# Kernel optimization log

Measured on AMD Instinct MI355X. Metric: run time of the kernel, lower is better.

## Reference

```python
import jax, jax.numpy as jnp
import numpy as np

B, N_ATOMS = 8192, 64      # molecules, atoms per molecule
DIM, EXTRA, N_CLS = 70, 7, 11
N_FP = 10000               # fingerprint vocab


def setup_inputs() -> dict:
    key = jax.random.key(0)
    ks = jax.random.split(key, 9)
    atoms = jax.random.randint(ks[0], (B, N_ATOMS), 0, N_FP, dtype=jnp.int64 if jax.config.jax_enable_x64 else jnp.int32)
    adjacency = jax.random.uniform(ks[1], (B, N_ATOMS, N_ATOMS), dtype=jnp.float32)
    sel_desc = jax.random.normal(ks[2], (B, EXTRA), dtype=jnp.float32)
    embed_table = jax.random.normal(ks[3], (N_FP, DIM), dtype=jnp.float32)
    w1 = jax.random.normal(ks[4], (DIM, DIM), dtype=jnp.float32) * 0.05
    b1 = jax.random.normal(ks[5], (DIM,), dtype=jnp.float32) * 0.05
    w2 = jax.random.normal(ks[6], (DIM, DIM), dtype=jnp.float32) * 0.05
    b2 = jax.random.normal(ks[7], (DIM,), dtype=jnp.float32) * 0.05
    wp = jax.random.normal(ks[8], (DIM + EXTRA, N_CLS), dtype=jnp.float32) * 0.05
    bp = jnp.zeros((N_CLS,), dtype=jnp.float32)
    return {"atoms": atoms, "adjacency": adjacency, "sel_desc": sel_desc,
            "embed_table": embed_table, "w1": w1, "b1": b1,
            "w2": w2, "b2": b2, "wp": wp, "bp": bp}


def reference(atoms, adjacency, sel_desc, embed_table, w1, b1, w2, b2, wp, bp):
    # embed atoms: [B, n, dim]
    x = embed_table[atoms]
    # message-passing layers: relu(linear) then (block-diagonal == batched) adjacency matmul
    for w, b in ((w1, b1), (w2, b2)):
        h = jax.nn.relu(jnp.einsum('bnd,de->bne', x, w) + b)
        x = jnp.einsum('bnm,bmd->bnd', adjacency, h)
    # segment-sum pool over atoms per molecule (sum_axis)
    y = jnp.sum(x, axis=1)                       # [B, dim]
    y = jnp.concatenate([y, sel_desc], axis=1)   # [B, dim+extra]
    return jnp.einsum('bd,dc->bc', y, wp) + bp   # [B, 11]
```

## Files before the change

kernel.cpp:

```cpp
#include <hip/hip_runtime.h>
#include <hip/hip_bf16.h>

#define NFP   10000
#define DIM   70
#define GPAD  72
#define NATOMS 64

typedef short  short8  __attribute__((ext_vector_type(8)));
typedef float  floatx4 __attribute__((ext_vector_type(4)));

__device__ inline unsigned short f2bf(float f) {
  union { float f; unsigned u; } x; x.f = f;
  unsigned r = x.u + 0x7fffu + ((x.u >> 16) & 1u);
  return (unsigned short)(r >> 16);
}

__device__ inline ushort2 pk2bf(float a, float b) {
  __hip_bfloat162 h = __float22bfloat162_rn(make_float2(a, b));
  union { __hip_bfloat162 h; ushort2 u; } c; c.h = h; return c.u;
}

__global__ __launch_bounds__(256) void precompute_G(
    const float* __restrict__ emb, const float* __restrict__ w1,
    const float* __restrict__ b1,  const float* __restrict__ w2,
    unsigned short* __restrict__ G) {
  __shared__ float w1s[DIM * GPAD];
  __shared__ float w2s[DIM * GPAD];
  __shared__ float b1s[GPAD];
  __shared__ float embs[32 * GPAD];
  __shared__ float e1s[32 * GPAD];
  const int t = threadIdx.x;

  for (int i = t; i < DIM * GPAD; i += 256) {
    int r = i / GPAD, c = i % GPAD;
    float v1 = 0.f, v2 = 0.f;
    if (c < DIM) { v1 = w1[r * DIM + c]; v2 = w2[r * DIM + c]; }
    w1s[i] = v1; w2s[i] = v2;
  }
  if (t < GPAD) b1s[t] = (t < DIM) ? b1[t] : 0.f;
  const int row0 = blockIdx.x * 32;
  for (int i = t; i < 32 * GPAD; i += 256) {
    int r = i / GPAD, c = i % GPAD;
    int vr = row0 + r;
    embs[i] = (vr < NFP && c < DIM) ? emb[vr * DIM + c] : 0.f;
  }
  __syncthreads();

  for (int task = t; task < 32 * 18; task += 256) {
    int r = task / 18, c4 = (task % 18) * 4;
    float4 acc = *(const float4*)&b1s[c4];
    for (int k = 0; k < DIM; k++) {
      float e = embs[r * GPAD + k];
      float4 w = *(const float4*)&w1s[k * GPAD + c4];
      acc.x = fmaf(e, w.x, acc.x); acc.y = fmaf(e, w.y, acc.y);
      acc.z = fmaf(e, w.z, acc.z); acc.w = fmaf(e, w.w, acc.w);
    }
    acc.x = fmaxf(acc.x, 0.f); acc.y = fmaxf(acc.y, 0.f);
    acc.z = fmaxf(acc.z, 0.f); acc.w = fmaxf(acc.w, 0.f);
    *(float4*)&e1s[r * GPAD + c4] = acc;
  }
  __syncthreads();

  for (int task = t; task < 32 * 18; task += 256) {
    int r = task / 18, c4 = (task % 18) * 4;
    int vr = row0 + r;
    if (vr >= NFP) continue;
    float ax = 0.f, ay = 0.f, az = 0.f, aw = 0.f;
    for (int k = 0; k < DIM; k++) {
      float e = e1s[r * GPAD + k];
      float4 w = *(const float4*)&w2s[k * GPAD + c4];
      ax = fmaf(e, w.x, ax); ay = fmaf(e, w.y, ay);
      az = fmaf(e, w.z, az); aw = fmaf(e, w.w, aw);
    }
    unsigned short* gp = G + vr * GPAD + c4;
    gp[0] = f2bf(ax); gp[1] = f2bf(ay); gp[2] = f2bf(az); gp[3] = f2bf(aw);
  }
}

__global__ __launch_bounds__(256, 6) void mol_fused(
    const int* __restrict__ atoms, const float* __restrict__ adj,
    const float* __restrict__ sel, const float* __restrict__ b2,
    const float* __restrict__ wp,  const float* __restrict__ bp,
    const unsigned short* __restrict__ G, float* __restrict__ out) {
  __shared__ unsigned short gTs[80 * GPAD];
  __shared__ float cpart[4 * 64];
  __shared__ float b2p[80];
  __shared__ float wps[77 * 11];
  __shared__ float bps[11];
  __shared__ float yacc[4 * 80];
  __shared__ float yv[80];

  const int b = blockIdx.x;
  const int t = threadIdx.x;
  const int w = t >> 6, lane = t & 63;
  const int q = lane >> 4, li = lane & 15;
  const int R = w * 16;

  const float* rp = adj + (size_t)b * 4096 + (R + li) * 64;
  float4 v0 = *(const float4*)(rp + q * 8);
  float4 v1 = *(const float4*)(rp + q * 8 + 4);
  float4 v2 = *(const float4*)(rp + 32 + q * 8);
  float4 v3 = *(const float4*)(rp + 36 + q * 8);
  union { short8 s; ushort2 u[4]; } A0, A1;
  A0.u[0] = pk2bf(v0.x, v0.y); A0.u[1] = pk2bf(v0.z, v0.w);
  A0.u[2] = pk2bf(v1.x, v1.y); A0.u[3] = pk2bf(v1.z, v1.w);
  A1.u[0] = pk2bf(v2.x, v2.y); A1.u[1] = pk2bf(v2.z, v2.w);
  A1.u[2] = pk2bf(v3.x, v3.y); A1.u[3] = pk2bf(v3.z, v3.w);
  {
    float c[16] = {v0.x, v0.y, v0.z, v0.w, v1.x, v1.y, v1.z, v1.w,
                   v2.x, v2.y, v2.z, v2.w, v3.x, v3.y, v3.z, v3.w};
#pragma unroll
    for (int m = 1; m <= 8; m <<= 1)
#pragma unroll
      for (int i = 0; i < 16; i++) c[i] += __shfl_xor(c[i], m);
    if (li == 0) {
      float* cp = &cpart[w * 64];
      *(float4*)&cp[q * 8]      = make_float4(c[0], c[1], c[2], c[3]);
      *(float4*)&cp[q * 8 + 4]  = make_float4(c[4], c[5], c[6], c[7]);
      *(float4*)&cp[32 + q * 8]     = make_float4(c[8],  c[9],  c[10], c[11]);
      *(float4*)&cp[32 + q * 8 + 4] = make_float4(c[12], c[13], c[14], c[15]);
    }
  }

  for (int i = t; i < 77 * 11; i += 256) wps[i] = wp[i];
  if (t < 11) bps[t] = bp[t];
  if (t < 80) b2p[t] = (t < DIM) ? b2[t] : 0.f;

  {
    const uint4* Gv = (const uint4*)G;
    const int p = t & 31;
    int2 aidx = *(const int2*)(atoms + b * 64 + 2 * p);
    int ch = t >> 5;
#pragma unroll
    for (int pass = 0; pass < 2; pass++) {
      if (pass == 1) { if (t >= 32) break; ch = 8; }
      uint4 g0 = Gv[(unsigned)aidx.x * 9 + ch];
      uint4 g1 = Gv[(unsigned)aidx.y * 9 + ch];
      unsigned base = (unsigned)(ch * 8) * GPAD + 2 * p;
      unsigned* d0 = (unsigned*)&gTs[base];
      d0[0 * (GPAD / 2) * 0] = 0;
      *(unsigned*)&gTs[base + 0 * GPAD] = (g0.x & 0xffffu) | (g1.x << 16);
      *(unsigned*)&gTs[base + 1 * GPAD] = (g0.x >> 16) | (g1.x & 0xffff0000u);
      *(unsigned*)&gTs[base + 2 * GPAD] = (g0.y & 0xffffu) | (g1.y << 16);
      *(unsigned*)&gTs[base + 3 * GPAD] = (g0.y >> 16) | (g1.y & 0xffff0000u);
      *(unsigned*)&gTs[base + 4 * GPAD] = (g0.z & 0xffffu) | (g1.z << 16);
      *(unsigned*)&gTs[base + 5 * GPAD] = (g0.z >> 16) | (g1.z & 0xffff0000u);
      *(unsigned*)&gTs[base + 6 * GPAD] = (g0.w & 0xffffu) | (g1.w << 16);
      *(unsigned*)&gTs[base + 7 * GPAD] = (g0.w >> 16) | (g1.w & 0xffff0000u);
    }
  }
  if (t < 72) {
    uint4 zz; zz.x = zz.y = zz.z = zz.w = 0u;
    *(uint4*)&gTs[72 * GPAD + t * 8] = zz;
  }
  __syncthreads();

  float cr[4];
#pragma unroll
  for (int r = 0; r < 4; r++) {
    int m = R + q * 4 + r;
    cr[r] = cpart[m] + cpart[64 + m] + cpart[128 + m] + cpart[192 + m];
  }

  floatx4 acc[5];
#pragma unroll
  for (int nt = 0; nt < 5; nt++) {
    floatx4 z = {0.f, 0.f, 0.f, 0.f};
    short8 b0 = *(const short8*)&gTs[(nt * 16 + li) * GPAD + q * 8];
    short8 b1 = *(const short8*)&gTs[(nt * 16 + li) * GPAD + 32 + q * 8];
    z = __builtin_amdgcn_mfma_f32_16x16x32_bf16(A0.s, b0, z, 0, 0, 0);
    z = __builtin_amdgcn_mfma_f32_16x16x32_bf16(A1.s, b1, z, 0, 0, 0);
    acc[nt] = z;
  }

  float ps[5];
#pragma unroll
  for (int nt = 0; nt < 5; nt++) {
    float bb = b2p[nt * 16 + li];
    float p = 0.f;
#pragma unroll
    for (int r = 0; r < 4; r++)
      p = fmaf(cr[r], fmaxf(acc[nt][r] + bb, 0.f), p);
    p += __shfl_xor(p, 16);
    p += __shfl_xor(p, 32);
    ps[nt] = p;
  }
  if (q == 0) {
#pragma unroll
    for (int nt = 0; nt < 5; nt++) yacc[w * 80 + nt * 16 + li] = ps[nt];
  }
  __syncthreads();

  if (t < 77) {
    float s;
    if (t < DIM) s = yacc[t] + yacc[80 + t] + yacc[160 + t] + yacc[240 + t];
    else         s = sel[(size_t)b * 7 + (t - DIM)];
    yv[t] = s;
  }
  __syncthreads();

  if (t < 11) {
    float s = bps[t];
#pragma unroll 7
    for (int d = 0; d < 77; d++) s = fmaf(yv[d], wps[d * 11 + t], s);
    out[(size_t)b * 11 + t] = s;
  }
}

extern "C" void kernel_launch(void* const* d_in, const int* in_sizes, int n_in,
                              void* d_out, int out_size, void* d_ws, size_t ws_size,
                              hipStream_t stream) {
  const int*   atoms = (const int*)d_in[0];
  const float* adj   = (const float*)d_in[1];
  const float* sel   = (const float*)d_in[2];
  const float* emb   = (const float*)d_in[3];
  const float* w1    = (const float*)d_in[4];
  const float* b1    = (const float*)d_in[5];
  const float* w2    = (const float*)d_in[6];
  const float* b2    = (const float*)d_in[7];
  const float* wp    = (const float*)d_in[8];
  const float* bp    = (const float*)d_in[9];

  const int B = in_sizes[0] / NATOMS;
  unsigned short* G = (unsigned short*)d_ws;

  precompute_G<<<(NFP + 31) / 32, 256, 0, stream>>>(emb, w1, b1, w2, G);
  mol_fused<<<B, 256, 0, stream>>>(atoms, adj, sel, b2, wp, bp, G, (float*)d_out);
}
```

Baseline: 260.0 us.

## Stage adjacency through LDS with coalesced loads and simplify gather and projection

The adjacency tile is now read with coalesced row-wise float4 loads, converted to bf16 and staged in shared memory, with column sums reduced via fewer shuffles. MFMA A operands are then read back from LDS. The G gather is restructured to one atom per lane with 16-bit LDS stores. The wp/bp projection weights are read directly from global memory instead of being staged. The precompute kernel uses 16 rows per block for more blocks, and the occupancy hint is removed. Together these aim to cut load latency and shuffle overhead, at the cost of extra LDS traffic and an extra barrier.

```diff
diff --git a/kernel.cpp b/kernel.cpp
--- a/kernel.cpp
+++ b/kernel.cpp
@@ -1,10 +1,11 @@
 #include <hip/hip_runtime.h>
 #include <hip/hip_bf16.h>
 
-#define NFP   10000
-#define DIM   70
-#define GPAD  72
+#define NFP    10000
+#define DIM    70
+#define GPAD   72
 #define NATOMS 64
+#define PGROWS 16
 
 typedef short  short8  __attribute__((ext_vector_type(8)));
 typedef float  floatx4 __attribute__((ext_vector_type(4)));
@@ -27,8 +28,8 @@
   __shared__ float w1s[DIM * GPAD];
   __shared__ float w2s[DIM * GPAD];
   __shared__ float b1s[GPAD];
-  __shared__ float embs[32 * GPAD];
-  __shared__ float e1s[32 * GPAD];
+  __shared__ float embs[PGROWS * GPAD];
+  __shared__ float e1s[PGROWS * GPAD];
   const int t = threadIdx.x;
 
   for (int i = t; i < DIM * GPAD; i += 256) {
@@ -38,15 +39,15 @@
     w1s[i] = v1; w2s[i] = v2;
   }
   if (t < GPAD) b1s[t] = (t < DIM) ? b1[t] : 0.f;
-  const int row0 = blockIdx.x * 32;
-  for (int i = t; i < 32 * GPAD; i += 256) {
+  const int row0 = blockIdx.x * PGROWS;
+  for (int i = t; i < PGROWS * GPAD; i += 256) {
     int r = i / GPAD, c = i % GPAD;
     int vr = row0 + r;
     embs[i] = (vr < NFP && c < DIM) ? emb[vr * DIM + c] : 0.f;
   }
   __syncthreads();
 
-  for (int task = t; task < 32 * 18; task += 256) {
+  for (int task = t; task < PGROWS * 18; task += 256) {
     int r = task / 18, c4 = (task % 18) * 4;
     float4 acc = *(const float4*)&b1s[c4];
     for (int k = 0; k < DIM; k++) {
@@ -61,7 +62,7 @@
   }
   __syncthreads();
 
-  for (int task = t; task < 32 * 18; task += 256) {
+  for (int task = t; task < PGROWS * 18; task += 256) {
     int r = task / 18, c4 = (task % 18) * 4;
     int vr = row0 + r;
     if (vr >= NFP) continue;
@@ -77,18 +78,18 @@
   }
 }
 
-__global__ __launch_bounds__(256, 6) void mol_fused(
+__global__ __launch_bounds__(256) void mol_fused(
     const int* __restrict__ atoms, const float* __restrict__ adj,
     const float* __restrict__ sel, const float* __restrict__ b2,
     const float* __restrict__ wp,  const float* __restrict__ bp,
     const unsigned short* __restrict__ G, float* __restrict__ out) {
+  __shared__ unsigned short adjs[64 * GPAD];
   __shared__ unsigned short gTs[80 * GPAD];
-  __shared__ float cpart[4 * 64];
+  __shared__ float cwave[4 * 64];
   __shared__ float b2p[80];
-  __shared__ float wps[77 * 11];
-  __shared__ float bps[11];
   __shared__ float yacc[4 * 80];
   __shared__ float yv[80];
+  __shared__ int   satoms[64];
 
   const int b = blockIdx.x;
   const int t = threadIdx.x;
@@ -96,57 +97,48 @@
   const int q = lane >> 4, li = lane & 15;
   const int R = w * 16;
 
-  const float* rp = adj + (size_t)b * 4096 + (R + li) * 64;
-  float4 v0 = *(const float4*)(rp + q * 8);
-  float4 v1 = *(const float4*)(rp + q * 8 + 4);
-  float4 v2 = *(const float4*)(rp + 32 + q * 8);
-  float4 v3 = *(const float4*)(rp + 36 + q * 8);
-  union { short8 s; ushort2 u[4]; } A0, A1;
-  A0.u[0] = pk2bf(v0.x, v0.y); A0.u[1] = pk2bf(v0.z, v0.w);
-  A0.u[2] = pk2bf(v1.x, v1.y); A0.u[3] = pk2bf(v1.z, v1.w);
-  A1.u[0] = pk2bf(v2.x, v2.y); A1.u[1] = pk2bf(v2.z, v2.w);
-  A1.u[2] = pk2bf(v3.x, v3.y); A1.u[3] = pk2bf(v3.z, v3.w);
+  if (t < 64) satoms[t] = atoms[b * 64 + t];
+  if (t < 80) b2p[t] = (t < DIM) ? b2[t] : 0.f;
+  __syncthreads();
+
   {
-    float c[16] = {v0.x, v0.y, v0.z, v0.w, v1.x, v1.y, v1.z, v1.w,
-                   v2.x, v2.y, v2.z, v2.w, v3.x, v3.y, v3.z, v3.w};
-#pragma unroll
-    for (int m = 1; m <= 8; m <<= 1)
-#pragma unroll
-      for (int i = 0; i < 16; i++) c[i] += __shfl_xor(c[i], m);
-    if (li == 0) {
-      float* cp = &cpart[w * 64];
-      *(float4*)&cp[q * 8]      = make_float4(c[0], c[1], c[2], c[3]);
-      *(float4*)&cp[q * 8 + 4]  = make_float4(c[4], c[5], c[6], c[7]);
-      *(float4*)&cp[32 + q * 8]     = make_float4(c[8],  c[9],  c[10], c[11]);
-      *(float4*)&cp[32 + q * 8 + 4] = make_float4(c[12], c[13], c[14], c[15]);
-    }
-  }
-
-  for (int i = t; i < 77 * 11; i += 256) wps[i] = wp[i];
-  if (t < 11) bps[t] = bp[t];
-  if (t < 80) b2p[t] = (t < DIM) ? b2[t] : 0.f;
+    const float* ap = adj + (size_t)b * 4096;
+    const int mc = (t & 15) * 4;
+    const int a  = t >> 4;
+    float4 cs = make_float4(0.f, 0.f, 0.f, 0.f);
+#pragma unroll
+    for (int it = 0; it < 4; it++) {
+      int n = a + 16 * it;
+      float4 v = *(const float4*)(ap + n * 64 + mc);
+      cs.x += v.x; cs.y += v.y; cs.z += v.z; cs.w += v.w;
+      ushort2 lo = pk2bf(v.x, v.y);
+      ushort2 hi = pk2bf(v.z, v.w);
+      ushort4 u; u.x = lo.x; u.y = lo.y; u.z = hi.x; u.w = hi.y;
+      *(ushort4*)&adjs[n * GPAD + mc] = u;
+    }
+#pragma unroll
+    for (int s = 16; s <= 32; s <<= 1) {
+      cs.x += __shfl_xor(cs.x, s); cs.y += __shfl_xor(cs.y, s);
+      cs.z += __shfl_xor(cs.z, s); cs.w += __shfl_xor(cs.w, s);
+    }
+    if (((t >> 4) & 3) == 0) *(float4*)&cwave[w * 64 + mc] = cs;
+  }
 
   {
+    const int m = t & 63;
+    const int row = satoms[m];
     const uint4* Gv = (const uint4*)G;
-    const int p = t & 31;
-    int2 aidx = *(const int2*)(atoms + b * 64 + 2 * p);
-    int ch = t >> 5;
-#pragma unroll
-    for (int pass = 0; pass < 2; pass++) {
-      if (pass == 1) { if (t >= 32) break; ch = 8; }
-      uint4 g0 = Gv[(unsigned)aidx.x * 9 + ch];
-      uint4 g1 = Gv[(unsigned)aidx.y * 9 + ch];
-      unsigned base = (unsigned)(ch * 8) * GPAD + 2 * p;
-      unsigned* d0 = (unsigned*)&gTs[base];
-      d0[0 * (GPAD / 2) * 0] = 0;
-      *(unsigned*)&gTs[base + 0 * GPAD] = (g0.x & 0xffffu) | (g1.x << 16);
-      *(unsigned*)&gTs[base + 1 * GPAD] = (g0.x >> 16) | (g1.x & 0xffff0000u);
-      *(unsigned*)&gTs[base + 2 * GPAD] = (g0.y & 0xffffu) | (g1.y << 16);
-      *(unsigned*)&gTs[base + 3 * GPAD] = (g0.y >> 16) | (g1.y & 0xffff0000u);
-      *(unsigned*)&gTs[base + 4 * GPAD] = (g0.z & 0xffffu) | (g1.z << 16);
-      *(unsigned*)&gTs[base + 5 * GPAD] = (g0.z >> 16) | (g1.z & 0xffff0000u);
-      *(unsigned*)&gTs[base + 6 * GPAD] = (g0.w & 0xffffu) | (g1.w << 16);
-      *(unsigned*)&gTs[base + 7 * GPAD] = (g0.w >> 16) | (g1.w & 0xffff0000u);
+    for (int ch = w; ch < 9; ch += 4) {
+      uint4 v = Gv[(unsigned)row * 9 + ch];
+      unsigned short* gp = &gTs[(ch * 8) * GPAD + m];
+      gp[0 * GPAD] = (unsigned short)(v.x & 0xffff);
+      gp[1 * GPAD] = (unsigned short)(v.x >> 16);
+      gp[2 * GPAD] = (unsigned short)(v.y & 0xffff);
+      gp[3 * GPAD] = (unsigned short)(v.y >> 16);
+      gp[4 * GPAD] = (unsigned short)(v.z & 0xffff);
+      gp[5 * GPAD] = (unsigned short)(v.z >> 16);
+      gp[6 * GPAD] = (unsigned short)(v.w & 0xffff);
+      gp[7 * GPAD] = (unsigned short)(v.w >> 16);
     }
   }
   if (t < 72) {
@@ -159,17 +151,19 @@
 #pragma unroll
   for (int r = 0; r < 4; r++) {
     int m = R + q * 4 + r;
-    cr[r] = cpart[m] + cpart[64 + m] + cpart[128 + m] + cpart[192 + m];
-  }
-
+    cr[r] = cwave[m] + cwave[64 + m] + cwave[128 + m] + cwave[192 + m];
+  }
+
+  short8 a0 = *(const short8*)&adjs[(R + li) * GPAD + q * 8];
+  short8 a1 = *(const short8*)&adjs[(R + li) * GPAD + 32 + q * 8];
   floatx4 acc[5];
 #pragma unroll
   for (int nt = 0; nt < 5; nt++) {
     floatx4 z = {0.f, 0.f, 0.f, 0.f};
     short8 b0 = *(const short8*)&gTs[(nt * 16 + li) * GPAD + q * 8];
     short8 b1 = *(const short8*)&gTs[(nt * 16 + li) * GPAD + 32 + q * 8];
-    z = __builtin_amdgcn_mfma_f32_16x16x32_bf16(A0.s, b0, z, 0, 0, 0);
-    z = __builtin_amdgcn_mfma_f32_16x16x32_bf16(A1.s, b1, z, 0, 0, 0);
+    z = __builtin_amdgcn_mfma_f32_16x16x32_bf16(a0, b0, z, 0, 0, 0);
+    z = __builtin_amdgcn_mfma_f32_16x16x32_bf16(a1, b1, z, 0, 0, 0);
     acc[nt] = z;
   }
 
@@ -200,9 +194,9 @@
   __syncthreads();
 
   if (t < 11) {
-    float s = bps[t];
-#pragma unroll 7
-    for (int d = 0; d < 77; d++) s = fmaf(yv[d], wps[d * 11 + t], s);
+    float s = bp[t];
+#pragma unroll 11
+    for (int d = 0; d < 77; d++) s = fmaf(yv[d], wp[d * 11 + t], s);
     out[(size_t)b * 11 + t] = s;
   }
 }
@@ -224,6 +218,6 @@
   const int B = in_sizes[0] / NATOMS;
   unsigned short* G = (unsigned short*)d_ws;
 
-  precompute_G<<<(NFP + 31) / 32, 256, 0, stream>>>(emb, w1, b1, w2, G);
+  precompute_G<<<(NFP + PGROWS - 1) / PGROWS, 256, 0, stream>>>(emb, w1, b1, w2, G);
   mol_fused<<<B, 256, 0, stream>>>(atoms, adj, sel, b2, wp, bp, G, (float*)d_out);
 }
```

Measured after the change: 244.0 us, median of 2. 1.07x faster.
